# Kernel tuning notes

Measured on AMD Instinct MI355X. Metric: run time of the kernel, lower is better.

## Reference

```python
import jax, jax.numpy as jnp
import numpy as np

D = 1024   # rnn_size
H = 64     # pooling MLP hidden
B, C = 16, 1024


def setup_inputs() -> dict:
    key = jax.random.key(0)
    ks = jax.random.split(key, 12)
    s = 1.0 / np.sqrt(D)
    inp = {
        "encoder_outputs": jax.random.normal(ks[0], (B, C, D), jnp.float32),
        # Linear weights stored as [in, out] (y = x @ W + b), same math as torch Linear
        "Wf": jax.random.uniform(ks[1], (D, D), jnp.float32, -s, s),
        "bf": jax.random.uniform(ks[2], (D,), jnp.float32, -s, s),
        "Wg": jax.random.uniform(ks[3], (D, D), jnp.float32, -s, s),
        "bg": jax.random.uniform(ks[4], (D,), jnp.float32, -s, s),
        "Wx": jax.random.uniform(ks[5], (D, D), jnp.float32, -s, s),
        "bx": jax.random.uniform(ks[6], (D,), jnp.float32, -s, s),
        "W1": jax.random.uniform(ks[7], (D, H), jnp.float32, -s, s),
        "b1": jax.random.uniform(ks[8], (H,), jnp.float32, -s, s),
        "W2": jax.random.uniform(ks[9], (H, 1), jnp.float32, -1.0 / np.sqrt(H), 1.0 / np.sqrt(H)),
        "b2": jax.random.uniform(ks[10], (1,), jnp.float32, -1.0 / np.sqrt(H), 1.0 / np.sqrt(H)),
        # gamma is nn.Parameter(zeros(1)); use a nonzero value for a nontrivial baseline
        "gamma": jax.random.normal(ks[11], (1,), jnp.float32) * 0.1,
    }
    return inp


def reference(encoder_outputs, Wf, bf, Wg, bg, Wx, bx, W1, b1, W2, b2, gamma):
    x = encoder_outputs                                  # [B, C, D]
    q = jax.nn.relu(x @ Wf + bf)                         # proj_query [B, C, D]
    k = jax.nn.relu(x @ Wg + bg)                         # proj_key   [B, C, D]
    v = jax.nn.relu(x @ Wx + bx)                         # proj_value [B, C, D]
    energy = jnp.einsum('bid,bjd->bij', q, k)            # [B, C, C]
    attn = jax.nn.softmax(energy, axis=1)                # softmax over dim=1 (non-standard axis)
    # out = attention^T @ v : out[b,j,d] = sum_i attn[b,i,j] * v[b,i,d]
    out = jnp.einsum('bij,bid->bjd', attn, v)            # [B, C, D]
    out = gamma * out + x                                # gamma-residual
    # MLP attention pooling over C
    e2 = jax.nn.relu(x @ W1 + b1) @ W2 + b2              # [B, C, 1]
    w = jax.nn.softmax(e2[..., 0], axis=1)               # [B, C]
    return jnp.sum(out * w[..., None], axis=1)           # [B, D]
```

## Files before the change

### kernel.cpp

```cpp
#include <hip/hip_runtime.h>

#define B_ 16
#define C_ 1024
#define D_ 1024
#define H_ 64
#define M_ (B_*C_)

typedef __attribute__((ext_vector_type(8))) short bf16x8;
typedef __attribute__((ext_vector_type(8))) unsigned short ushortx8;
typedef __attribute__((ext_vector_type(4))) float f32x4;

__device__ __forceinline__ float wave_max(float v){
  #pragma unroll
  for (int o = 32; o > 0; o >>= 1) v = fmaxf(v, __shfl_xor(v, o));
  return v;
}
__device__ __forceinline__ float wave_sum(float v){
  #pragma unroll
  for (int o = 32; o > 0; o >>= 1) v += __shfl_xor(v, o);
  return v;
}

__device__ __forceinline__ ushort f2bf(float f){
  union { float f; unsigned u; } a; a.f = f;
  unsigned r = a.u + 0x7fff + ((a.u >> 16) & 1);
  return (ushort)(r >> 16);
}
__device__ __forceinline__ float bf2f(ushort h){
  union { unsigned u; float f; } a; a.u = ((unsigned)h) << 16; return a.f;
}

__device__ __forceinline__ void lds_cp16(const ushort* g, ushort* l){
  __builtin_amdgcn_global_load_lds(
      (const __attribute__((address_space(1))) void*)g,
      (__attribute__((address_space(3))) void*)l, 16, 0, 0);
}

__device__ __forceinline__ int fsw(int row){
  return (row & 3) ^ ((row >> 2) & 3);
}


__global__ __launch_bounds__(256) void cvt_kernel(
    const float* __restrict__ in, ushort* __restrict__ out, int n4)
{
  int i = blockIdx.x*256 + threadIdx.x;
  if (i >= n4) return;
  float4 v = ((const float4*)in)[i];
  ushort4 o;
  o.x = f2bf(v.x); o.y = f2bf(v.y); o.z = f2bf(v.z); o.w = f2bf(v.w);
  ((ushort4*)out)[i] = o;
}

__global__ __launch_bounds__(256) void tconv3_kernel(
    const float* __restrict__ Wf, const float* __restrict__ Wg,
    const float* __restrict__ Wx, ushort* __restrict__ Wt)
{
  __shared__ float tile[32][33];
  const int z = blockIdx.z;
  const float* W = (z == 0) ? Wf : (z == 1) ? Wg : Wx;
  ushort* Out = Wt + (size_t)z*D_*D_;
  const int t = threadIdx.x;
  const int tx = t & 31, ty = t >> 5;
  const int n0 = blockIdx.x*32, k0 = blockIdx.y*32;
  #pragma unroll
  for (int i = 0; i < 32; i += 8)
    tile[ty+i][tx] = W[(size_t)(k0+ty+i)*D_ + n0+tx];
  __syncthreads();
  #pragma unroll
  for (int i = 0; i < 32; i += 8)
    Out[(size_t)(n0+ty+i)*D_ + k0+tx] = f2bf(tile[tx][ty+i]);
}

__global__ __launch_bounds__(256) void tconv64_kernel(
    const float* __restrict__ W1, ushort* __restrict__ W1t)
{
  __shared__ float tile[32][33];
  const int t = threadIdx.x;
  const int tx = t & 31, ty = t >> 5;
  const int n0 = blockIdx.x*32, k0 = blockIdx.y*32;
  #pragma unroll
  for (int i = 0; i < 32; i += 8)
    tile[ty+i][tx] = W1[(size_t)(k0+ty+i)*H_ + n0+tx];
  __syncthreads();
  #pragma unroll
  for (int i = 0; i < 32; i += 8)
    W1t[(size_t)(n0+ty+i)*D_ + k0+tx] = f2bf(tile[tx][ty+i]);
}

__global__ __launch_bounds__(256) void proj_kernel(
    const ushort* __restrict__ A, const ushort* __restrict__ Wt,
    const float* __restrict__ bf, const float* __restrict__ bg,
    const float* __restrict__ bx,
    ushort* __restrict__ q, ushort* __restrict__ k, ushort* __restrict__ v)
{
  __shared__ ushort As[128*32];
  __shared__ ushort Bs[128*32];
  const int t = threadIdx.x;
  const int wid = t >> 6, lane = t & 63;
  const int m0 = blockIdx.y * 128, n0 = blockIdx.x * 128;
  const int seg = n0 >> 10;
  const int nloc0 = n0 - (seg << 10);

  const int r = t >> 2;
  const int kc = ((t & 3) ^ fsw(r)) * 8;
  const ushort* ga0 = A + (size_t)(m0 + r)*1024 + kc;
  const ushort* ga1 = ga0 + (size_t)64*1024;
  const ushort* gb0 = Wt + (size_t)(n0 + r)*1024 + kc;
  const ushort* gb1 = gb0 + (size_t)64*1024;
  ushort* lA = As + wid*512;
  ushort* lB = Bs + wid*512;

  const int quad = lane >> 4, l16 = lane & 15;
  const int wm = wid >> 1, wn = wid & 1;
  const int fr = fsw(l16);
  const int am0 = (wm*64 + l16)*32 + ((quad ^ fr)*8);
  const int bn0 = (wn*64 + l16)*32 + ((quad ^ fr)*8);

  f32x4 acc[4][4] = {};

  for (int k0 = 0; k0 < 1024; k0 += 32) {
    lds_cp16(ga0, lA); lds_cp16(ga1, lA + 2048);
    lds_cp16(gb0, lB); lds_cp16(gb1, lB + 2048);
    ga0 += 32; ga1 += 32; gb0 += 32; gb1 += 32;
    __syncthreads();
    bf16x8 af[4], bfr[4];
    #pragma unroll
    for (int i = 0; i < 4; ++i) {
      af[i]  = *(const bf16x8*)&As[am0 + i*512];
      bfr[i] = *(const bf16x8*)&Bs[bn0 + i*512];
    }
    #pragma unroll
    for (int mt = 0; mt < 4; ++mt)
      #pragma unroll
      for (int nt = 0; nt < 4; ++nt)
        acc[mt][nt] = __builtin_amdgcn_mfma_f32_16x16x32_bf16(
            af[mt], bfr[nt], acc[mt][nt], 0, 0, 0);
    __syncthreads();
  }

  const float* bp = (seg == 0) ? bf : (seg == 1) ? bg : bx;
  ushort* op      = (seg == 0) ? q  : (seg == 1) ? k  : v;
  const int gm_base = m0 + wm*64 + quad*4;
  const int gn_base = nloc0 + wn*64 + l16;
  float bv[4];
  #pragma unroll
  for (int nt = 0; nt < 4; ++nt) bv[nt] = bp[gn_base + nt*16];
  #pragma unroll
  for (int mt = 0; mt < 4; ++mt)
    #pragma unroll
    for (int rr = 0; rr < 4; ++rr) {
      const size_t rowoff = (size_t)(gm_base + mt*16 + rr) * 1024;
      #pragma unroll
      for (int nt = 0; nt < 4; ++nt)
        op[rowoff + gn_base + nt*16] =
            f2bf(fmaxf(acc[mt][nt][rr] + bv[nt], 0.f));
    }
}

__global__ __launch_bounds__(256) void energy_kernel(
    const ushort* __restrict__ Km, const ushort* __restrict__ Qm,
    ushort* __restrict__ E)
{
  __shared__ ushort As[128*32];
  __shared__ ushort Bs[128*32];
  const int t = threadIdx.x;
  const int wid = t >> 6, lane = t & 63;
  const int m0 = blockIdx.y * 128, n0 = blockIdx.x * 128;
  const ushort* Ab = Km + (size_t)blockIdx.z * C_ * D_;
  const ushort* Bb = Qm + (size_t)blockIdx.z * C_ * D_;

  const int r = t >> 2;
  const int kc = ((t & 3) ^ fsw(r)) * 8;
  const ushort* ga0 = Ab + (size_t)(m0 + r)*1024 + kc;
  const ushort* ga1 = ga0 + (size_t)64*1024;
  const ushort* gb0 = Bb + (size_t)(n0 + r)*1024 + kc;
  const ushort* gb1 = gb0 + (size_t)64*1024;
  ushort* lA = As + wid*512;
  ushort* lB = Bs + wid*512;

  const int quad = lane >> 4, l16 = lane & 15;
  const int wm = wid >> 1, wn = wid & 1;
  const int fr = fsw(l16);
  const int am0 = (wm*64 + l16)*32 + ((quad ^ fr)*8);
  const int bn0 = (wn*64 + l16)*32 + ((quad ^ fr)*8);

  f32x4 acc[4][4] = {};

  for (int k0 = 0; k0 < 1024; k0 += 32) {
    lds_cp16(ga0, lA); lds_cp16(ga1, lA + 2048);
    lds_cp16(gb0, lB); lds_cp16(gb1, lB + 2048);
    ga0 += 32; ga1 += 32; gb0 += 32; gb1 += 32;
    __syncthreads();
    bf16x8 af[4], bfr[4];
    #pragma unroll
    for (int i = 0; i < 4; ++i) {
      af[i]  = *(const bf16x8*)&As[am0 + i*512];
      bfr[i] = *(const bf16x8*)&Bs[bn0 + i*512];
    }
    #pragma unroll
    for (int mt = 0; mt < 4; ++mt)
      #pragma unroll
      for (int nt = 0; nt < 4; ++nt)
        acc[mt][nt] = __builtin_amdgcn_mfma_f32_16x16x32_bf16(
            af[mt], bfr[nt], acc[mt][nt], 0, 0, 0);
    __syncthreads();
  }

  ushort* O = E + (size_t)blockIdx.z * C_ * C_;
  const int gm_base = m0 + wm*64 + quad*4;
  const int gn_base = n0 + wn*64 + l16;
  #pragma unroll
  for (int mt = 0; mt < 4; ++mt)
    #pragma unroll
    for (int rr = 0; rr < 4; ++rr) {
      const size_t rowoff = (size_t)(gm_base + mt*16 + rr) * 1024;
      #pragma unroll
      for (int nt = 0; nt < 4; ++nt)
        O[rowoff + gn_base + nt*16] = f2bf(acc[mt][nt][rr]);
    }
}

__global__ __launch_bounds__(256) void pool_mfma_kernel(
    const ushort* __restrict__ A, const ushort* __restrict__ Bt,
    const float* __restrict__ b1, const float* __restrict__ W2,
    float* __restrict__ e2out)
{
  __shared__ ushort As[128*32];
  __shared__ ushort Bs[64*32];
  const int t = threadIdx.x;
  const int wid = t >> 6, lane = t & 63;
  const int m0 = blockIdx.x * 128;

  const int r = t >> 2;
  const int kc = ((t & 3) ^ fsw(r)) * 8;
  const ushort* ga0 = A + (size_t)(m0 + r)*1024 + kc;
  const ushort* ga1 = ga0 + (size_t)64*1024;
  const ushort* gb0 = Bt + (size_t)r*1024 + kc;
  ushort* lA = As + wid*512;
  ushort* lB = Bs + wid*512;

  const int quad = lane >> 4, l16 = lane & 15;
  const int fr = fsw(l16);
  const int am0 = (wid*32 + l16)*32 + ((quad ^ fr)*8);
  const int bn0 = l16*32 + ((quad ^ fr)*8);

  f32x4 acc[2][4] = {};

  for (int k0 = 0; k0 < 1024; k0 += 32) {
    lds_cp16(ga0, lA); lds_cp16(ga1, lA + 2048);
    lds_cp16(gb0, lB);
    ga0 += 32; ga1 += 32; gb0 += 32;
    __syncthreads();
    bf16x8 af[2], bfr[4];
    #pragma unroll
    for (int i = 0; i < 2; ++i) af[i] = *(const bf16x8*)&As[am0 + i*512];
    #pragma unroll
    for (int i = 0; i < 4; ++i) bfr[i] = *(const bf16x8*)&Bs[bn0 + i*512];
    #pragma unroll
    for (int mt = 0; mt < 2; ++mt)
      #pragma unroll
      for (int nt = 0; nt < 4; ++nt)
        acc[mt][nt] = __builtin_amdgcn_mfma_f32_16x16x32_bf16(
            af[mt], bfr[nt], acc[mt][nt], 0, 0, 0);
    __syncthreads();
  }

  float b1v[4], w2v[4];
  #pragma unroll
  for (int nt = 0; nt < 4; ++nt) {
    b1v[nt] = b1[nt*16 + l16];
    w2v[nt] = W2[nt*16 + l16];
  }
  #pragma unroll
  for (int mt = 0; mt < 2; ++mt)
    #pragma unroll
    for (int rr = 0; rr < 4; ++rr) {
      float h = 0.f;
      #pragma unroll
      for (int nt = 0; nt < 4; ++nt)
        h += fmaxf(acc[mt][nt][rr] + b1v[nt], 0.f) * w2v[nt];
      #pragma unroll
      for (int o = 1; o < 16; o <<= 1) h += __shfl_xor(h, o);
      if (l16 == 0)
        e2out[m0 + wid*32 + mt*16 + quad*4 + rr] = h;
    }
}


__global__ __launch_bounds__(256) void fused_sm_kernel(
    const ushort* __restrict__ E, const float* __restrict__ w,
    float* __restrict__ u_part)
{
  __shared__ float ul[4][1024];
  const int b = blockIdx.y;
  const int strip = blockIdx.x;
  const int t = threadIdx.x, wv = t >> 6, lane = t & 63;
  const ushort* Eb = E + (size_t)b*C_*C_;
  const float* wb = w + (size_t)b*C_;
  float acc[2][8] = {};
  #pragma unroll
  for (int rj = 0; rj < 4; ++rj) {
    const int j = strip*16 + wv*4 + rj;
    const ushort* row = Eb + (size_t)j*C_;
    float vv[2][8];
    float m = -1e30f;
    #pragma unroll
    for (int c = 0; c < 2; ++c) {
      ushortx8 h = *(const ushortx8*)&row[c*512 + lane*8];
      #pragma unroll
      for (int kk = 0; kk < 8; ++kk) {
        vv[c][kk] = bf2f(h[kk]);
        m = fmaxf(m, vv[c][kk]);
      }
    }
    m = wave_max(m);
    float e[2][8];
    float s = 0.f;
    #pragma unroll
    for (int c = 0; c < 2; ++c)
      #pragma unroll
      for (int kk = 0; kk < 8; ++kk) {
        e[c][kk] = expf(vv[c][kk] - m);
        s += e[c][kk];
      }
    s = wave_sum(s);
    const float sc = wb[j] / s;
    #pragma unroll
    for (int c = 0; c < 2; ++c)
      #pragma unroll
      for (int kk = 0; kk < 8; ++kk) acc[c][kk] += sc * e[c][kk];
  }
  #pragma unroll
  for (int c = 0; c < 2; ++c)
    #pragma unroll
    for (int k4 = 0; k4 < 2; ++k4) {
      float4 o;
      o.x = acc[c][k4*4+0]; o.y = acc[c][k4*4+1];
      o.z = acc[c][k4*4+2]; o.w = acc[c][k4*4+3];
      *(float4*)&ul[wv][c*512 + lane*8 + k4*4] = o;
    }
  __syncthreads();
  float4 r0 = *(float4*)&ul[0][t*4];
  float4 r1 = *(float4*)&ul[1][t*4];
  float4 r2 = *(float4*)&ul[2][t*4];
  float4 r3 = *(float4*)&ul[3][t*4];
  float4 o;
  o.x = r0.x+r1.x+r2.x+r3.x; o.y = r0.y+r1.y+r2.y+r3.y;
  o.z = r0.z+r1.z+r2.z+r3.z; o.w = r0.w+r1.w+r2.w+r3.w;
  *(float4*)&u_part[((size_t)strip*B_ + b)*C_ + t*4] = o;
}

__global__ __launch_bounds__(256) void u_combine_kernel(
    const float* __restrict__ u_part, float* __restrict__ u)
{
  const int idx = blockIdx.x*256 + threadIdx.x;
  float s = 0.f;
  #pragma unroll 8
  for (int sp = 0; sp < 64; ++sp) s += u_part[(size_t)sp*B_*C_ + idx];
  u[idx] = s;
}


__global__ __launch_bounds__(256) void softmax_w_kernel(
    const float* __restrict__ e2in, float* __restrict__ w)
{
  __shared__ float redm[4];
  __shared__ float reds[4];
  const int b = blockIdx.x, t = threadIdx.x;
  const int lane = t & 63, wid = t >> 6;
  const float* row = e2in + (size_t)b*C_;
  float4 v = *(const float4*)&row[t*4];
  float m = fmaxf(fmaxf(v.x, v.y), fmaxf(v.z, v.w));
  m = wave_max(m);
  if (lane == 0) redm[wid] = m;
  __syncthreads();
  m = fmaxf(fmaxf(redm[0], redm[1]), fmaxf(redm[2], redm[3]));
  float e0 = expf(v.x - m), e1 = expf(v.y - m);
  float e2 = expf(v.z - m), e3 = expf(v.w - m);
  float s = e0 + e1 + e2 + e3;
  s = wave_sum(s);
  if (lane == 0) reds[wid] = s;
  __syncthreads();
  s = reds[0] + reds[1] + reds[2] + reds[3];
  const float inv = 1.0f / s;
  float4 o; o.x = e0*inv; o.y = e1*inv; o.z = e2*inv; o.w = e3*inv;
  *(float4*)&w[(size_t)b*C_ + t*4] = o;
}


__global__ __launch_bounds__(256) void final_part_kernel(
    const ushort* __restrict__ X, const ushort* __restrict__ V,
    const float* __restrict__ u, const float* __restrict__ w,
    const float* __restrict__ gamma, float* __restrict__ fpart)
{
  const int b = blockIdx.x, s = blockIdx.y;
  const int d0 = threadIdx.x * 4;
  const ushort* xb = X + (size_t)b*C_*D_;
  const ushort* vb = V + (size_t)b*C_*D_;
  const float* ub = u + (size_t)b*C_;
  const float* wb = w + (size_t)b*C_;
  float4 av = {0,0,0,0}, ax = {0,0,0,0};
  #pragma unroll
  for (int ii = 0; ii < 16; ++ii) {
    const int i = s*16 + ii;
    const float ui = ub[i], wi = wb[i];
    ushort4 vv = *(const ushort4*)&vb[(size_t)i*D_ + d0];
    ushort4 xv = *(const ushort4*)&xb[(size_t)i*D_ + d0];
    av.x += ui*bf2f(vv.x); av.y += ui*bf2f(vv.y);
    av.z += ui*bf2f(vv.z); av.w += ui*bf2f(vv.w);
    ax.x += wi*bf2f(xv.x); ax.y += wi*bf2f(xv.y);
    ax.z += wi*bf2f(xv.z); ax.w += wi*bf2f(xv.w);
  }
  const float g = gamma[0];
  float4 o;
  o.x = g*av.x + ax.x; o.y = g*av.y + ax.y;
  o.z = g*av.z + ax.z; o.w = g*av.w + ax.w;
  *(float4*)&fpart[((size_t)s*B_ + b)*D_ + d0] = o;
}

__global__ __launch_bounds__(256) void final_combine_kernel(
    const float* __restrict__ fpart, float* __restrict__ out)
{
  const int idx = blockIdx.x*256 + threadIdx.x;
  float s = 0.f;
  #pragma unroll 8
  for (int sp = 0; sp < 64; ++sp) s += fpart[(size_t)sp*B_*D_ + idx];
  out[idx] = s;
}

extern "C" void kernel_launch(void* const* d_in, const int* in_sizes, int n_in,
                              void* d_out, int out_size, void* d_ws, size_t ws_size,
                              hipStream_t stream) {
  (void)in_sizes; (void)n_in; (void)out_size; (void)ws_size;
  const float* x  = (const float*)d_in[0];
  const float* Wf = (const float*)d_in[1];
  const float* bf = (const float*)d_in[2];
  const float* Wg = (const float*)d_in[3];
  const float* bg = (const float*)d_in[4];
  const float* Wx = (const float*)d_in[5];
  const float* bx = (const float*)d_in[6];
  const float* W1 = (const float*)d_in[7];
  const float* b1 = (const float*)d_in[8];
  const float* W2 = (const float*)d_in[9];
  const float* gamma = (const float*)d_in[11];
  float* out = (float*)d_out;

  ushort* x_bf = (ushort*)d_ws;
  ushort* wt   = x_bf + (size_t)M_*D_;
  ushort* w1t  = wt + (size_t)3*D_*D_;
  ushort* q_bf = w1t + (size_t)H_*D_;
  ushort* k_bf = q_bf + (size_t)M_*D_;
  ushort* v_bf = k_bf + (size_t)M_*D_;
  ushort* E    = v_bf + (size_t)M_*D_;
  float*  e2b  = (float*)(E + (size_t)B_*C_*C_);
  float*  wbuf = e2b + M_;
  float*  u    = wbuf + M_;
  float*  u_part = u + M_;
  float*  fpart  = u_part;

  cvt_kernel<<<dim3((M_*D_/4 + 255)/256), 256, 0, stream>>>(x, x_bf, M_*D_/4);
  tconv3_kernel<<<dim3(32,32,3), 256, 0, stream>>>(Wf, Wg, Wx, wt);
  tconv64_kernel<<<dim3(2,32), 256, 0, stream>>>(W1, w1t);

  proj_kernel<<<dim3(24,128), 256, 0, stream>>>(x_bf, wt, bf, bg, bx,
                                                q_bf, k_bf, v_bf);

  pool_mfma_kernel<<<dim3(M_/128), 256, 0, stream>>>(x_bf, w1t, b1, W2, e2b);
  softmax_w_kernel<<<dim3(B_), 256, 0, stream>>>(e2b, wbuf);

  energy_kernel<<<dim3(8,8,B_), 256, 0, stream>>>(k_bf, q_bf, E);
  fused_sm_kernel<<<dim3(64,B_), 256, 0, stream>>>(E, wbuf, u_part);
  u_combine_kernel<<<dim3(M_/256), 256, 0, stream>>>(u_part, u);

  final_part_kernel<<<dim3(B_,64), 256, 0, stream>>>(x_bf, v_bf, u, wbuf, gamma, fpart);
  final_combine_kernel<<<dim3(M_/256), 256, 0, stream>>>(fpart, out);
}
```

Before: 360.3 us.

## Merge prep kernels, load GEMM B operand directly to registers, fold u-combine into final

Combines the x conversion and the three weight transpose kernels into a single prep launch. In the projection and energy GEMMs, the B operand is now read from global memory straight into registers instead of being staged through LDS, which halves LDS use and the LDS traffic per block. The separate u_combine kernel is removed, and each final_part block sums its own 64 partial u values through shared memory. The direct B loads have a non-swizzled global access pattern and nothing hides their latency, which could stall the MFMA loop.

```diff
diff --git a/kernel.cpp b/kernel.cpp
--- a/kernel.cpp
+++ b/kernel.cpp
@@ -40,52 +40,48 @@
   return (row & 3) ^ ((row >> 2) & 3);
 }
 
-
-__global__ __launch_bounds__(256) void cvt_kernel(
-    const float* __restrict__ in, ushort* __restrict__ out, int n4)
-{
-  int i = blockIdx.x*256 + threadIdx.x;
-  if (i >= n4) return;
-  float4 v = ((const float4*)in)[i];
-  ushort4 o;
-  o.x = f2bf(v.x); o.y = f2bf(v.y); o.z = f2bf(v.z); o.w = f2bf(v.w);
-  ((ushort4*)out)[i] = o;
-}
-
-__global__ __launch_bounds__(256) void tconv3_kernel(
-    const float* __restrict__ Wf, const float* __restrict__ Wg,
-    const float* __restrict__ Wx, ushort* __restrict__ Wt)
+__global__ __launch_bounds__(256) void prep_kernel(
+    const float* __restrict__ x, const float* __restrict__ Wf,
+    const float* __restrict__ Wg, const float* __restrict__ Wx,
+    const float* __restrict__ W1,
+    ushort* __restrict__ x_bf, ushort* __restrict__ wt,
+    ushort* __restrict__ w1t)
 {
   __shared__ float tile[32][33];
-  const int z = blockIdx.z;
-  const float* W = (z == 0) ? Wf : (z == 1) ? Wg : Wx;
-  ushort* Out = Wt + (size_t)z*D_*D_;
+  const int blk = blockIdx.x;
   const int t = threadIdx.x;
-  const int tx = t & 31, ty = t >> 5;
-  const int n0 = blockIdx.x*32, k0 = blockIdx.y*32;
-  #pragma unroll
-  for (int i = 0; i < 32; i += 8)
-    tile[ty+i][tx] = W[(size_t)(k0+ty+i)*D_ + n0+tx];
-  __syncthreads();
-  #pragma unroll
-  for (int i = 0; i < 32; i += 8)
-    Out[(size_t)(n0+ty+i)*D_ + k0+tx] = f2bf(tile[tx][ty+i]);
-}
-
-__global__ __launch_bounds__(256) void tconv64_kernel(
-    const float* __restrict__ W1, ushort* __restrict__ W1t)
-{
-  __shared__ float tile[32][33];
-  const int t = threadIdx.x;
-  const int tx = t & 31, ty = t >> 5;
-  const int n0 = blockIdx.x*32, k0 = blockIdx.y*32;
-  #pragma unroll
-  for (int i = 0; i < 32; i += 8)
-    tile[ty+i][tx] = W1[(size_t)(k0+ty+i)*H_ + n0+tx];
-  __syncthreads();
-  #pragma unroll
-  for (int i = 0; i < 32; i += 8)
-    W1t[(size_t)(n0+ty+i)*D_ + k0+tx] = f2bf(tile[tx][ty+i]);
+  if (blk < 16384) {
+    const int i = blk*256 + t;
+    float4 v = ((const float4*)x)[i];
+    ushort4 o;
+    o.x = f2bf(v.x); o.y = f2bf(v.y); o.z = f2bf(v.z); o.w = f2bf(v.w);
+    ((ushort4*)x_bf)[i] = o;
+  } else if (blk < 16384 + 3072) {
+    const int bb = blk - 16384;
+    const int z = bb >> 10, rem = bb & 1023;
+    const int n0 = (rem & 31)*32, k0 = (rem >> 5)*32;
+    const float* W = (z == 0) ? Wf : (z == 1) ? Wg : Wx;
+    ushort* Out = wt + (size_t)z*D_*D_;
+    const int tx = t & 31, ty = t >> 5;
+    #pragma unroll
+    for (int i = 0; i < 32; i += 8)
+      tile[ty+i][tx] = W[(size_t)(k0+ty+i)*D_ + n0+tx];
+    __syncthreads();
+    #pragma unroll
+    for (int i = 0; i < 32; i += 8)
+      Out[(size_t)(n0+ty+i)*D_ + k0+tx] = f2bf(tile[tx][ty+i]);
+  } else {
+    const int bb = blk - 16384 - 3072;
+    const int n0 = (bb & 1)*32, k0 = (bb >> 1)*32;
+    const int tx = t & 31, ty = t >> 5;
+    #pragma unroll
+    for (int i = 0; i < 32; i += 8)
+      tile[ty+i][tx] = W1[(size_t)(k0+ty+i)*H_ + n0+tx];
+    __syncthreads();
+    #pragma unroll
+    for (int i = 0; i < 32; i += 8)
+      w1t[(size_t)(n0+ty+i)*D_ + k0+tx] = f2bf(tile[tx][ty+i]);
+  }
 }
 
 __global__ __launch_bounds__(256) void proj_kernel(
@@ -95,7 +91,6 @@
     ushort* __restrict__ q, ushort* __restrict__ k, ushort* __restrict__ v)
 {
   __shared__ ushort As[128*32];
-  __shared__ ushort Bs[128*32];
   const int t = threadIdx.x;
   const int wid = t >> 6, lane = t & 63;
   const int m0 = blockIdx.y * 128, n0 = blockIdx.x * 128;
@@ -106,30 +101,33 @@
   const int kc = ((t & 3) ^ fsw(r)) * 8;
   const ushort* ga0 = A + (size_t)(m0 + r)*1024 + kc;
   const ushort* ga1 = ga0 + (size_t)64*1024;
-  const ushort* gb0 = Wt + (size_t)(n0 + r)*1024 + kc;
-  const ushort* gb1 = gb0 + (size_t)64*1024;
   ushort* lA = As + wid*512;
-  ushort* lB = Bs + wid*512;
 
   const int quad = lane >> 4, l16 = lane & 15;
   const int wm = wid >> 1, wn = wid & 1;
   const int fr = fsw(l16);
   const int am0 = (wm*64 + l16)*32 + ((quad ^ fr)*8);
-  const int bn0 = (wn*64 + l16)*32 + ((quad ^ fr)*8);
+
+  const ushort* gB0 = Wt + (size_t)(n0 + wn*64 +  0 + l16)*1024 + quad*8;
+  const ushort* gB1 = Wt + (size_t)(n0 + wn*64 + 16 + l16)*1024 + quad*8;
+  const ushort* gB2 = Wt + (size_t)(n0 + wn*64 + 32 + l16)*1024 + quad*8;
+  const ushort* gB3 = Wt + (size_t)(n0 + wn*64 + 48 + l16)*1024 + quad*8;
 
   f32x4 acc[4][4] = {};
 
   for (int k0 = 0; k0 < 1024; k0 += 32) {
     lds_cp16(ga0, lA); lds_cp16(ga1, lA + 2048);
-    lds_cp16(gb0, lB); lds_cp16(gb1, lB + 2048);
-    ga0 += 32; ga1 += 32; gb0 += 32; gb1 += 32;
-    __syncthreads();
-    bf16x8 af[4], bfr[4];
-    #pragma unroll
-    for (int i = 0; i < 4; ++i) {
-      af[i]  = *(const bf16x8*)&As[am0 + i*512];
-      bfr[i] = *(const bf16x8*)&Bs[bn0 + i*512];
-    }
+    ga0 += 32; ga1 += 32;
+    bf16x8 bfr[4];
+    bfr[0] = *(const bf16x8*)gB0; gB0 += 32;
+    bfr[1] = *(const bf16x8*)gB1; gB1 += 32;
+    bfr[2] = *(const bf16x8*)gB2; gB2 += 32;
+    bfr[3] = *(const bf16x8*)gB3; gB3 += 32;
+    __syncthreads();
+    bf16x8 af[4];
+    #pragma unroll
+    for (int i = 0; i < 4; ++i)
+      af[i] = *(const bf16x8*)&As[am0 + i*512];
     #pragma unroll
     for (int mt = 0; mt < 4; ++mt)
       #pragma unroll
@@ -163,7 +161,6 @@
     ushort* __restrict__ E)
 {
   __shared__ ushort As[128*32];
-  __shared__ ushort Bs[128*32];
   const int t = threadIdx.x;
   const int wid = t >> 6, lane = t & 63;
   const int m0 = blockIdx.y * 128, n0 = blockIdx.x * 128;
@@ -174,30 +171,33 @@
   const int kc = ((t & 3) ^ fsw(r)) * 8;
   const ushort* ga0 = Ab + (size_t)(m0 + r)*1024 + kc;
   const ushort* ga1 = ga0 + (size_t)64*1024;
-  const ushort* gb0 = Bb + (size_t)(n0 + r)*1024 + kc;
-  const ushort* gb1 = gb0 + (size_t)64*1024;
   ushort* lA = As + wid*512;
-  ushort* lB = Bs + wid*512;
 
   const int quad = lane >> 4, l16 = lane & 15;
   const int wm = wid >> 1, wn = wid & 1;
   const int fr = fsw(l16);
   const int am0 = (wm*64 + l16)*32 + ((quad ^ fr)*8);
-  const int bn0 = (wn*64 + l16)*32 + ((quad ^ fr)*8);
+
+  const ushort* gB0 = Bb + (size_t)(n0 + wn*64 +  0 + l16)*1024 + quad*8;
+  const ushort* gB1 = Bb + (size_t)(n0 + wn*64 + 16 + l16)*1024 + quad*8;
+  const ushort* gB2 = Bb + (size_t)(n0 + wn*64 + 32 + l16)*1024 + quad*8;
+  const ushort* gB3 = Bb + (size_t)(n0 + wn*64 + 48 + l16)*1024 + quad*8;
 
   f32x4 acc[4][4] = {};
 
   for (int k0 = 0; k0 < 1024; k0 += 32) {
     lds_cp16(ga0, lA); lds_cp16(ga1, lA + 2048);
-    lds_cp16(gb0, lB); lds_cp16(gb1, lB + 2048);
-    ga0 += 32; ga1 += 32; gb0 += 32; gb1 += 32;
-    __syncthreads();
-    bf16x8 af[4], bfr[4];
-    #pragma unroll
-    for (int i = 0; i < 4; ++i) {
-      af[i]  = *(const bf16x8*)&As[am0 + i*512];
-      bfr[i] = *(const bf16x8*)&Bs[bn0 + i*512];
-    }
+    ga0 += 32; ga1 += 32;
+    bf16x8 bfr[4];
+    bfr[0] = *(const bf16x8*)gB0; gB0 += 32;
+    bfr[1] = *(const bf16x8*)gB1; gB1 += 32;
+    bfr[2] = *(const bf16x8*)gB2; gB2 += 32;
+    bfr[3] = *(const bf16x8*)gB3; gB3 += 32;
+    __syncthreads();
+    bf16x8 af[4];
+    #pragma unroll
+    for (int i = 0; i < 4; ++i)
+      af[i] = *(const bf16x8*)&As[am0 + i*512];
     #pragma unroll
     for (int mt = 0; mt < 4; ++mt)
       #pragma unroll
@@ -286,7 +286,6 @@
         e2out[m0 + wid*32 + mt*16 + quad*4 + rr] = h;
     }
 }
-
 
 __global__ __launch_bounds__(256) void fused_sm_kernel(
     const ushort* __restrict__ E, const float* __restrict__ w,
@@ -350,17 +349,6 @@
   o.z = r0.z+r1.z+r2.z+r3.z; o.w = r0.w+r1.w+r2.w+r3.w;
   *(float4*)&u_part[((size_t)strip*B_ + b)*C_ + t*4] = o;
 }
-
-__global__ __launch_bounds__(256) void u_combine_kernel(
-    const float* __restrict__ u_part, float* __restrict__ u)
-{
-  const int idx = blockIdx.x*256 + threadIdx.x;
-  float s = 0.f;
-  #pragma unroll 8
-  for (int sp = 0; sp < 64; ++sp) s += u_part[(size_t)sp*B_*C_ + idx];
-  u[idx] = s;
-}
-
 
 __global__ __launch_bounds__(256) void softmax_w_kernel(
     const float* __restrict__ e2in, float* __restrict__ w)
@@ -388,23 +376,43 @@
   *(float4*)&w[(size_t)b*C_ + t*4] = o;
 }
 
-
 __global__ __launch_bounds__(256) void final_part_kernel(
     const ushort* __restrict__ X, const ushort* __restrict__ V,
-    const float* __restrict__ u, const float* __restrict__ w,
+    const float* __restrict__ u_part, const float* __restrict__ w,
     const float* __restrict__ gamma, float* __restrict__ fpart)
 {
   const int b = blockIdx.x, s = blockIdx.y;
-  const int d0 = threadIdx.x * 4;
+  const int t = threadIdx.x;
+  __shared__ float red[16][17];
+  __shared__ float us[16];
+  {
+    const int ii = t & 15, g = t >> 4;
+    float p = 0.f;
+    #pragma unroll
+    for (int q2 = 0; q2 < 4; ++q2) {
+      const int sp = g*4 + q2;
+      p += u_part[((size_t)sp*B_ + b)*C_ + s*16 + ii];
+    }
+    red[ii][g] = p;
+  }
+  __syncthreads();
+  if (t < 16) {
+    float s2 = 0.f;
+    #pragma unroll
+    for (int g = 0; g < 16; ++g) s2 += red[t][g];
+    us[t] = s2;
+  }
+  __syncthreads();
+
+  const int d0 = t * 4;
   const ushort* xb = X + (size_t)b*C_*D_;
   const ushort* vb = V + (size_t)b*C_*D_;
-  const float* ub = u + (size_t)b*C_;
   const float* wb = w + (size_t)b*C_;
   float4 av = {0,0,0,0}, ax = {0,0,0,0};
   #pragma unroll
   for (int ii = 0; ii < 16; ++ii) {
     const int i = s*16 + ii;
-    const float ui = ub[i], wi = wb[i];
+    const float ui = us[ii], wi = wb[i];
     ushort4 vv = *(const ushort4*)&vb[(size_t)i*D_ + d0];
     ushort4 xv = *(const ushort4*)&xb[(size_t)i*D_ + d0];
     av.x += ui*bf2f(vv.x); av.y += ui*bf2f(vv.y);
@@ -455,13 +463,11 @@
   ushort* E    = v_bf + (size_t)M_*D_;
   float*  e2b  = (float*)(E + (size_t)B_*C_*C_);
   float*  wbuf = e2b + M_;
-  float*  u    = wbuf + M_;
-  float*  u_part = u + M_;
-  float*  fpart  = u_part;
-
-  cvt_kernel<<<dim3((M_*D_/4 + 255)/256), 256, 0, stream>>>(x, x_bf, M_*D_/4);
-  tconv3_kernel<<<dim3(32,32,3), 256, 0, stream>>>(Wf, Wg, Wx, wt);
-  tconv64_kernel<<<dim3(2,32), 256, 0, stream>>>(W1, w1t);
+  float*  u_part = wbuf + M_;
+  float*  fpart  = (float*)E;
+
+  prep_kernel<<<dim3(16384+3072+64), 256, 0, stream>>>(
+      x, Wf, Wg, Wx, W1, x_bf, wt, w1t);
 
   proj_kernel<<<dim3(24,128), 256, 0, stream>>>(x_bf, wt, bf, bg, bx,
                                                 q_bf, k_bf, v_bf);
@@ -471,8 +477,8 @@
 
   energy_kernel<<<dim3(8,8,B_), 256, 0, stream>>>(k_bf, q_bf, E);
   fused_sm_kernel<<<dim3(64,B_), 256, 0, stream>>>(E, wbuf, u_part);
-  u_combine_kernel<<<dim3(M_/256), 256, 0, stream>>>(u_part, u);
-
-  final_part_kernel<<<dim3(B_,64), 256, 0, stream>>>(x_bf, v_bf, u, wbuf, gamma, fpart);
+
+  final_part_kernel<<<dim3(B_,64), 256, 0, stream>>>(x_bf, v_bf, u_part, wbuf,
+                                                     gamma, fpart);
   final_combine_kernel<<<dim3(M_/256), 256, 0, stream>>>(fpart, out);
 }
```

Measured after the change: 459.8 us. +27.6%, slower.
